# Performance work log

Hardware: AMD Instinct MI355X
Metric: run time of the kernel (lower is better)

## Reference

```python
import jax, jax.numpy as jnp
import numpy as np

BN_EPS = 1e-5
POOL_EPS = 1e-6


def conv3x3(x, w, b):
    # x: (N,C,H,W), w: (O,C,3,3) -> (N,O,H,W), stride 1, SAME padding
    y = jax.lax.conv_general_dilated(x, w, window_strides=(1, 1), padding='SAME',
                                     dimension_numbers=('NCHW', 'OIHW', 'NCHW'))
    return y + b[None, :, None, None]


def deform_conv2d(x, off_w, off_b, mod_w, mod_b, w, b):
    # Modulated deformable conv (DCNv2), 3x3, stride 1, padding 1 (torchvision semantics).
    N, C, H, W = x.shape
    off = conv3x3(x, off_w, off_b).reshape(N, 9, 2, H, W)  # per-tap (dy, dx)
    mod = 2.0 * jax.nn.sigmoid(conv3x3(x, mod_w, mod_b))   # (N,9,H,W)
    dy = (jnp.arange(3, dtype=x.dtype) - 1.0).repeat(3)    # tap k = ky*3+kx
    dx = jnp.tile(jnp.arange(3, dtype=x.dtype) - 1.0, 3)
    py = off[:, :, 0] + dy[None, :, None, None] + jnp.arange(H, dtype=x.dtype)[None, None, :, None]
    px = off[:, :, 1] + dx[None, :, None, None] + jnp.arange(W, dtype=x.dtype)[None, None, None, :]
    y0f = jnp.floor(py); x0f = jnp.floor(px)
    wy = py - y0f; wx = px - x0f
    y0 = y0f.astype(jnp.int32); x0 = x0f.astype(jnp.int32)
    flat = x.reshape(N, C, H * W)

    def gather(yi, xi):
        # zero padding outside the image
        valid = ((yi >= 0) & (yi < H) & (xi >= 0) & (xi < W)).astype(x.dtype)
        idx = jnp.clip(yi, 0, H - 1) * W + jnp.clip(xi, 0, W - 1)      # (N,9,H,W)
        idx_b = jnp.broadcast_to(idx.reshape(N, 1, -1), (N, C, 9 * H * W))
        g = jnp.take_along_axis(flat, idx_b, axis=2).reshape(N, C, 9, H, W)
        return g * valid[:, None]

    s = (gather(y0, x0) * ((1 - wy) * (1 - wx))[:, None]
         + gather(y0, x0 + 1) * ((1 - wy) * wx)[:, None]
         + gather(y0 + 1, x0) * (wy * (1 - wx))[:, None]
         + gather(y0 + 1, x0 + 1) * (wy * wx)[:, None])       # (N,C,9,H,W)
    out = jnp.einsum('nckij,nkij,ock->noij', s, mod, w.reshape(w.shape[0], C, 9))
    return out + b[None, :, None, None]


def setup_inputs() -> dict:
    key = jax.random.key(0)
    ks = jax.random.split(key, 20)
    b, n_f, n_i, Hm, Wm = 2, 8, 10, 192, 192
    C_in, C_dcn, n_inc, n_pix = 256, 64, 128, 64
    h, w = 96, 96
    f32 = jnp.float32
    inp = {
        'x': jax.random.normal(ks[0], (b * n_f, C_in, h, w), f32),
        'masks': jax.random.uniform(ks[1], (b, n_f, n_i, Hm, Wm), f32),
        'conv1_w': jax.random.normal(ks[2], (C_dcn, C_in, 3, 3), f32) * 0.02,
        'conv1_b': jnp.zeros((C_dcn,), f32),
        'bn_gamma': jnp.ones((C_dcn,), f32),
        'bn_beta': jnp.zeros((C_dcn,), f32),
        'bn_mean': jax.random.normal(ks[3], (C_dcn,), f32) * 0.01,
        'bn_var': jnp.ones((C_dcn,), f32),
        'off_w': jax.random.normal(ks[4], (18, C_dcn, 3, 3), f32) * 0.01,
        'off_b': jnp.zeros((18,), f32),
        'mod_w': jax.random.normal(ks[5], (9, C_dcn, 3, 3), f32) * 0.01,
        'mod_b': jnp.zeros((9,), f32),
        'dcn_w': jax.random.normal(ks[6], (C_dcn, C_dcn, 3, 3), f32) * 0.05,
        'dcn_b': jnp.zeros((C_dcn,), f32),
        'smooth_w': jax.random.normal(ks[7], (C_dcn, C_dcn), f32) * 0.05,
        'smooth_b': jnp.zeros((C_dcn,), f32),
        'inc_w': jax.random.normal(ks[8], (n_inc, C_dcn), f32) * 0.05,
        'pix_w': jax.random.normal(ks[9], (n_pix, C_dcn), f32) * 0.05,
    }
    return inp


def reference(x, masks, conv1_w, conv1_b, bn_gamma, bn_beta, bn_mean, bn_var,
              off_w, off_b, mod_w, mod_b, dcn_w, dcn_b,
              smooth_w, smooth_b, inc_w, pix_w):
    # conv1: Conv3x3 + BatchNorm (eval stats) + ReLU
    y = conv3x3(x, conv1_w, conv1_b)
    y = (y - bn_mean[None, :, None, None]) * (bn_gamma[None, :, None, None]
        * jax.lax.rsqrt(bn_var + BN_EPS)[None, :, None, None]) + bn_beta[None, :, None, None]
    y = jax.nn.relu(y)
    # deformable conv
    y = deform_conv2d(y, off_w, off_b, mod_w, mod_b, dcn_w, dcn_b)

    b, n_f, n_i, Hm, Wm = masks.shape
    N, C, h, w = y.shape
    # resizeAnyShape -> bilinear, align_corners=False
    m = jax.image.resize(masks.reshape(b * n_f * n_i, Hm, Wm),
                         (b * n_f * n_i, h, w), method='bilinear', antialias=False)
    m = m.reshape(b, n_f, n_i, h * w)
    xf = y.reshape(b, n_f, C, h * w)
    # mask-weighted spatial average: avoid (b,n_f,n_i,C,h*w) intermediate
    num = jnp.einsum('bfcp,bfip->bfic', xf, m)            # (b,n_f,n_i,C)
    den = m.sum(axis=-1)[..., None]                        # (b,n_f,n_i,1)
    feat = num / (den + POOL_EPS)
    feat = jax.nn.relu(feat @ smooth_w.T + smooth_b)
    inc_kernels = feat @ inc_w.T
    pix_kernels = feat @ pix_w.T
    return (inc_kernels, pix_kernels)
```

## Files before the change

### kernel.cpp

```cpp
#include <hip/hip_runtime.h>
#include <hip/hip_bf16.h>

typedef __attribute__((ext_vector_type(8))) __bf16 bf16x8;
typedef __attribute__((ext_vector_type(4))) float f32x4;
typedef __attribute__((ext_vector_type(4))) unsigned int u32x4;
typedef __attribute__((ext_vector_type(2))) unsigned int u32x2;
typedef __attribute__((ext_vector_type(4))) unsigned short u16x4;
typedef __attribute__((ext_vector_type(8))) unsigned short ushort8;

#define MFMA16(a,b,c) __builtin_amdgcn_mfma_f32_16x16x32_bf16((a),(b),(c),0,0,0)

__device__ __forceinline__ float b2f(unsigned short u) {
  union { unsigned int i; float f; } v; v.i = ((unsigned int)u) << 16; return v.f;
}
__device__ __forceinline__ unsigned short f2b(float f) {
  union { float f; unsigned int u; } v; v.f = f;
  unsigned int u = v.u;
  unsigned int r = (u + 0x7fffu + ((u >> 16) & 1u)) >> 16;
  return (unsigned short)r;
}
__device__ __forceinline__ unsigned short f2h(float f) {
  _Float16 x = (_Float16)f; unsigned short r; __builtin_memcpy(&r, &x, 2); return r;
}
__device__ __forceinline__ float h2f(unsigned short h) {
  _Float16 x; __builtin_memcpy(&x, &h, 2); return (float)x;
}

#define NIMG 16
#define CIN  256
#define CD   64
#define HH   96
#define WW   96
#define HW   (HH*WW)

#define OFF_Y1   (0ll)
#define OFF_Y2   (18874368ll)
#define OFF_OFF  (37748736ll)
#define OFF_MOD  (48365568ll)
#define OFF_M    (53673984ll)
#define OFF_NP   OFF_OFF
#define OFF_DP   (OFF_OFF + 1310720ll)
#define OFF_SBN  (59908096ll)
#define OFF_TBN  (59908352ll)
#define OFF_W1   (59908608ll)
#define OFF_W2   (60203520ll)
#define OFF_W3   (60240384ll)
#define WS_NEEDED (60314112ll)

__global__ void k_prep(const float* __restrict__ conv1_w, const float* __restrict__ conv1_b,
                       const float* __restrict__ bn_gamma, const float* __restrict__ bn_beta,
                       const float* __restrict__ bn_mean, const float* __restrict__ bn_var,
                       const float* __restrict__ off_w, const float* __restrict__ mod_w,
                       const float* __restrict__ dcn_w,
                       unsigned short* __restrict__ w1, unsigned short* __restrict__ w2,
                       unsigned short* __restrict__ w3,
                       float* __restrict__ sbn, float* __restrict__ tbn)
{
  int e = blockIdx.x * 256 + threadIdx.x;
  if (e < 147456) {
    int j = e & 7, o = (e >> 3) & 63, cg = (e >> 9) & 31, t = e >> 14;
    w1[e] = f2b(conv1_w[(o * 256 + cg * 8 + j) * 9 + t]);
  } else if (e < 147456 + 18432) {
    int i = e - 147456;
    int j = i & 7, o = (i >> 3) & 31, cg = (i >> 8) & 7, t = i >> 11;
    int ch = cg * 8 + j;
    float v = 0.f;
    if (o < 18)      v = off_w[(o * 64 + ch) * 9 + t];
    else if (o < 27) v = mod_w[((o - 18) * 64 + ch) * 9 + t];
    w2[i] = f2b(v);
  } else if (e < 147456 + 18432 + 36864) {
    int i = e - 147456 - 18432;
    int j = i & 7, o = (i >> 3) & 63, cg = (i >> 9) & 7, t = i >> 12;
    w3[i] = f2b(dcn_w[(o * 64 + cg * 8 + j) * 9 + t]);
  } else {
    int i = e - (147456 + 18432 + 36864);
    if (i < 64) {
      sbn[i] = bn_gamma[i] * rsqrtf(bn_var[i] + 1e-5f);
    } else if (i < 128) {
      int q = i - 64;
      float s = bn_gamma[q] * rsqrtf(bn_var[q] + 1e-5f);
      tbn[q] = (conv1_b[q] - bn_mean[q]) * s + bn_beta[q];
    }
  }
}

__global__ __launch_bounds__(256)
void k_tr(const float* __restrict__ x, unsigned short* __restrict__ xT, int n_base)
{
  __shared__ __align__(16) unsigned short ls[64][68];
  const int tid = threadIdx.x;
  const int p0 = blockIdx.x * 64, c0 = blockIdx.y * 64, nl = blockIdx.z;
  const float* xn = x + (size_t)(n_base + nl) * CIN * HW;

  const int p4 = tid & 15, cb = tid >> 4;
  #pragma unroll
  for (int it = 0; it < 4; ++it) {
    int c = cb + it * 16;
    f32x4 v = *reinterpret_cast<const f32x4*>(xn + (size_t)(c0 + c) * HW + p0 + p4 * 4);
    #pragma unroll
    for (int q = 0; q < 4; ++q) ls[p4 * 4 + q][c] = f2b(v[q]);
  }
  __syncthreads();
  const int cg = tid & 7, pb = tid >> 3;
  #pragma unroll
  for (int it = 0; it < 2; ++it) {
    int p = pb + it * 32;
    u32x2 lo = *reinterpret_cast<const u32x2*>(&ls[p][cg * 8]);
    u32x2 hi = *reinterpret_cast<const u32x2*>(&ls[p][cg * 8 + 4]);
    u32x4 v = {lo[0], lo[1], hi[0], hi[1]};
    *reinterpret_cast<u32x4*>(&xT[((size_t)nl * HW + p0 + p) * CIN + c0 + cg * 8]) = v;
  }
}

__global__ __launch_bounds__(256)
void k_conv1t(const unsigned short* __restrict__ xT, const unsigned short* __restrict__ w1,
              const float* __restrict__ sbn, const float* __restrict__ tbn,
              unsigned short* __restrict__ y1, int n_base)
{
  __shared__ __align__(16) unsigned short xs[4][98][40];

  const int tid = threadIdx.x;
  const int lane = tid & 63, wv = tid >> 6;
  const int l16 = lane & 15, lg = lane >> 4;
  const int wrow = wv & 1, wch = wv >> 1;
  const int h0 = blockIdx.x * 2;
  const int nl = blockIdx.y;
  const int n = n_base + nl;
  const unsigned short* xn = xT + (size_t)nl * HW * CIN;

  f32x4 acc[2][6];
  #pragma unroll
  for (int a = 0; a < 2; ++a)
    #pragma unroll
    for (int b = 0; b < 6; ++b) { f32x4 z = {0.f,0.f,0.f,0.f}; acc[a][b] = z; }

  for (int chunk = 0; chunk < 8; ++chunk) {
    const int c0 = chunk * 32;
    __syncthreads();
    #pragma unroll
    for (int it = 0; it < 6; ++it) {
      int idx = tid + it * 256;
      int cg = idx & 3, w = (idx >> 2) % 96, r = idx / 384;
      int row = h0 - 1 + r;
      u32x4 v = {0u,0u,0u,0u};
      if (row >= 0 && row < HH)
        v = *reinterpret_cast<const u32x4*>(&xn[((size_t)row * WW + w) * CIN + c0 + cg * 8]);
      *reinterpret_cast<u32x4*>(&xs[r][w + 1][cg * 8]) = v;
    }
    if (tid < 32) {
      int r = tid >> 3, side = (tid >> 2) & 1, cg = tid & 3;
      u32x4 z = {0u,0u,0u,0u};
      *reinterpret_cast<u32x4*>(&xs[r][side * 97][cg * 8]) = z;
    }
    __syncthreads();
    #pragma unroll
    for (int t = 0; t < 9; ++t) {
      const int ky = t / 3, kx = t % 3;
      bf16x8 a0 = *reinterpret_cast<const bf16x8*>(
          &w1[((t * 32 + chunk * 4 + lg) * 64 + wch * 32 + l16) * 8]);
      bf16x8 a1 = *reinterpret_cast<const bf16x8*>(
          &w1[((t * 32 + chunk * 4 + lg) * 64 + wch * 32 + 16 + l16) * 8]);
      const int r = wrow + ky;
      #pragma unroll
      for (int wt = 0; wt < 6; ++wt) {
        bf16x8 b = *reinterpret_cast<const bf16x8*>(&xs[r][wt*16 + l16 + kx][lg*8]);
        acc[0][wt] = MFMA16(a0, b, acc[0][wt]);
        acc[1][wt] = MFMA16(a1, b, acc[1][wt]);
      }
    }
  }
  __syncthreads();
  unsigned short* ys = &xs[0][0][0];
  #pragma unroll
  for (int ct = 0; ct < 2; ++ct) {
    int o4 = wch * 32 + ct * 16 + lg * 4;
    f32x4 s4 = *reinterpret_cast<const f32x4*>(&sbn[o4]);
    f32x4 t4 = *reinterpret_cast<const f32x4*>(&tbn[o4]);
    #pragma unroll
    for (int wt = 0; wt < 6; ++wt) {
      int p = wrow * 96 + wt * 16 + l16;
      float v0 = acc[ct][wt][0] * s4[0] + t4[0]; v0 = v0 > 0.f ? v0 : 0.f;
      float v1 = acc[ct][wt][1] * s4[1] + t4[1]; v1 = v1 > 0.f ? v1 : 0.f;
      float v2 = acc[ct][wt][2] * s4[2] + t4[2]; v2 = v2 > 0.f ? v2 : 0.f;
      float v3 = acc[ct][wt][3] * s4[3] + t4[3]; v3 = v3 > 0.f ? v3 : 0.f;
      u32x2 d = {(unsigned)f2b(v0) | ((unsigned)f2b(v1) << 16),
                 (unsigned)f2b(v2) | ((unsigned)f2b(v3) << 16)};
      *reinterpret_cast<u32x2*>(&ys[p * 72 + o4]) = d;
    }
  }
  __syncthreads();
  #pragma unroll
  for (int it = 0; it < 6; ++it) {
    int idx = tid + it * 256;
    int cg = idx & 7, p = (idx >> 3) % 96, r = idx / 768;
    *reinterpret_cast<u32x4*>(&y1[(((size_t)n * HH + h0 + r) * WW + p) * CD + cg * 8]) =
      *reinterpret_cast<const u32x4*>(&ys[(r * 96 + p) * 72 + cg * 8]);
  }
}

__global__ __launch_bounds__(256)
void k_conv2(const unsigned short* __restrict__ y1, const unsigned short* __restrict__ w2,
             const float* __restrict__ off_b, const float* __restrict__ mod_b,
             float* __restrict__ off_o, float* __restrict__ mod_o)
{
  __shared__ __align__(16) unsigned short xs[4][98][40];

  const int tid = threadIdx.x;
  const int lane = tid & 63, wv = tid >> 6;
  const int l16 = lane & 15, lg = lane >> 4;
  const int wrow = wv & 1, wct = wv >> 1;
  const int h0 = blockIdx.x * 2;
  const int n = blockIdx.y;
  const unsigned short* y1n = y1 + (size_t)n * HW * CD;

  f32x4 acc[6];
  #pragma unroll
  for (int b = 0; b < 6; ++b) { f32x4 z = {0.f,0.f,0.f,0.f}; acc[b] = z; }

  #pragma unroll
  for (int chunk = 0; chunk < 2; ++chunk) {
    const int c0 = chunk * 32;
    bf16x8 aR[9];
    #pragma unroll
    for (int t = 0; t < 9; ++t)
      aR[t] = *reinterpret_cast<const bf16x8*>(
          &w2[((t * 8 + chunk * 4 + lg) * 32 + wct * 16 + l16) * 8]);
    __syncthreads();
    #pragma unroll
    for (int it = 0; it < 6; ++it) {
      int idx = tid + it * 256;
      int cg = idx & 3, w = (idx >> 2) % 96, r = idx / 384;
      int row = h0 - 1 + r;
      u32x4 v = {0u,0u,0u,0u};
      if (row >= 0 && row < HH)
        v = *reinterpret_cast<const u32x4*>(&y1n[((size_t)row * WW + w) * CD + c0 + cg * 8]);
      *reinterpret_cast<u32x4*>(&xs[r][w + 1][cg * 8]) = v;
    }
    if (tid < 32) {
      int r = tid >> 3, side = (tid >> 2) & 1, cg = tid & 3;
      u32x4 z = {0u,0u,0u,0u};
      *reinterpret_cast<u32x4*>(&xs[r][side * 97][cg * 8]) = z;
    }
    __syncthreads();
    #pragma unroll
    for (int t = 0; t < 9; ++t) {
      const int ky = t / 3, kx = t % 3;
      const int r = wrow + ky;
      #pragma unroll
      for (int wt = 0; wt < 6; ++wt) {
        bf16x8 b = *reinterpret_cast<const bf16x8*>(&xs[r][wt*16 + l16 + kx][lg*8]);
        acc[wt] = MFMA16(aR[t], b, acc[wt]);
      }
    }
  }
  const int h = h0 + wrow;
  #pragma unroll
  for (int j = 0; j < 4; ++j) {
    int o = wct * 16 + lg * 4 + j;
    if (o < 18) {
      float bo = off_b[o];
      #pragma unroll
      for (int wt = 0; wt < 6; ++wt)
        off_o[((n * 18 + o) * HH + h) * WW + wt * 16 + l16] = acc[wt][j] + bo;
    } else if (o < 27) {
      int q = o - 18;
      float bo = mod_b[q];
      #pragma unroll
      for (int wt = 0; wt < 6; ++wt) {
        float v = acc[wt][j] + bo;
        mod_o[((n * 9 + q) * HH + h) * WW + wt * 16 + l16] = 2.f / (1.f + expf(-v));
      }
    }
  }
}

__global__ __launch_bounds__(256)
void k_dcn(const unsigned short* __restrict__ y1, const float* __restrict__ off_i,
           const float* __restrict__ mod_i, const unsigned short* __restrict__ w3g,
           const float* __restrict__ dcn_b, unsigned short* __restrict__ y2)
{
  __shared__ __align__(16) unsigned short meta[864][8];
  __shared__ __align__(16) unsigned short Bs[96][72];

  const int tid = threadIdx.x;
  const int lane = tid & 63, wv = tid >> 6;
  const int l16 = lane & 15, lg = lane >> 4;
  const int h = blockIdx.x, n = blockIdx.y;

  #pragma unroll
  for (int it = 0; it < 4; ++it) {
    int e = tid + it * 256;
    if (e < 864) {
      int k = e / 96, p = e % 96;
      float dy = off_i[((n * 18 + 2 * k) * HH + h) * WW + p];
      float dx = off_i[((n * 18 + 2 * k + 1) * HH + h) * WW + p];
      float mw = mod_i[((n * 9 + k) * HH + h) * WW + p];
      float py = (float)(h + k / 3 - 1) + dy;
      float px = (float)(p + k % 3 - 1) + dx;
      float y0f = floorf(py), x0f = floorf(px);
      float wy = py - y0f, wx = px - x0f;
      int iy0 = (int)y0f, ix0 = (int)x0f;
      int iy1 = iy0 + 1, ix1 = ix0 + 1;
      float vy0 = (iy0 >= 0 && iy0 < HH) ? 1.f : 0.f;
      float vy1 = (iy1 >= 0 && iy1 < HH) ? 1.f : 0.f;
      float vx0 = (ix0 >= 0 && ix0 < WW) ? 1.f : 0.f;
      float vx1 = (ix1 >= 0 && ix1 < WW) ? 1.f : 0.f;
      unsigned short m0 = f2h((1.f - wy) * (1.f - wx) * mw * vy0 * vx0);
      unsigned short m1 = f2h((1.f - wy) * wx         * mw * vy0 * vx1);
      unsigned short m2 = f2h(wy         * (1.f - wx) * mw * vy1 * vx0);
      unsigned short m3 = f2h(wy         * wx         * mw * vy1 * vx1);
      int cy0 = iy0 < 0 ? 0 : (iy0 > 95 ? 95 : iy0);
      int cy1 = iy1 < 0 ? 0 : (iy1 > 95 ? 95 : iy1);
      int cx0 = ix0 < 0 ? 0 : (ix0 > 95 ? 95 : ix0);
      int cx1 = ix1 < 0 ? 0 : (ix1 > 95 ? 95 : ix1);
      u32x4 pk = {(unsigned)m0 | ((unsigned)m1 << 16),
                  (unsigned)m2 | ((unsigned)m3 << 16),
                  (unsigned)(cy0 * WW + cx0) | ((unsigned)(cy0 * WW + cx1) << 16),
                  (unsigned)(cy1 * WW + cx0) | ((unsigned)(cy1 * WW + cx1) << 16)};
      *reinterpret_cast<u32x4*>(&meta[e][0]) = pk;
    }
  }
  __syncthreads();

  const unsigned short* y1n = y1 + (size_t)n * HW * CD;
  f32x4 acc[6];
  #pragma unroll
  for (int b = 0; b < 6; ++b) { f32x4 z = {0.f,0.f,0.f,0.f}; acc[b] = z; }

  #pragma unroll
  for (int t = 0; t < 9; ++t) {
    bf16x8 a0 = *reinterpret_cast<const bf16x8*>(
        &w3g[((t * 8 + lg) * 64 + wv * 16 + l16) * 8]);
    bf16x8 a1 = *reinterpret_cast<const bf16x8*>(
        &w3g[((t * 8 + 4 + lg) * 64 + wv * 16 + l16) * 8]);
    #pragma unroll
    for (int it = 0; it < 3; ++it) {
      int idx = tid + it * 256;
      int cg = idx & 7, p = idx >> 3;
      u32x4 mk = *reinterpret_cast<const u32x4*>(&meta[t * 96 + p][0]);
      float hw0 = h2f((unsigned short)(mk[0] & 0xffffu));
      float hw1 = h2f((unsigned short)(mk[0] >> 16));
      float hw2 = h2f((unsigned short)(mk[1] & 0xffffu));
      float hw3 = h2f((unsigned short)(mk[1] >> 16));
      int o0 = (int)(mk[2] & 0xffffu) << 6;
      int o1 = (int)(mk[2] >> 16) << 6;
      int o2 = (int)(mk[3] & 0xffffu) << 6;
      int o3 = (int)(mk[3] >> 16) << 6;
      ushort8 g0 = *reinterpret_cast<const ushort8*>(&y1n[o0 + cg * 8]);
      ushort8 g1 = *reinterpret_cast<const ushort8*>(&y1n[o1 + cg * 8]);
      ushort8 g2 = *reinterpret_cast<const ushort8*>(&y1n[o2 + cg * 8]);
      ushort8 g3 = *reinterpret_cast<const ushort8*>(&y1n[o3 + cg * 8]);
      unsigned int wds[4];
      #pragma unroll
      for (int q = 0; q < 4; ++q) {
        float va = hw0*b2f(g0[2*q])   + hw1*b2f(g1[2*q])
                 + hw2*b2f(g2[2*q])   + hw3*b2f(g3[2*q]);
        float vb = hw0*b2f(g0[2*q+1]) + hw1*b2f(g1[2*q+1])
                 + hw2*b2f(g2[2*q+1]) + hw3*b2f(g3[2*q+1]);
        wds[q] = (unsigned int)f2b(va) | ((unsigned int)f2b(vb) << 16);
      }
      u32x4 pk = {wds[0], wds[1], wds[2], wds[3]};
      *reinterpret_cast<u32x4*>(&Bs[p][cg * 8]) = pk;
    }
    __syncthreads();
    #pragma unroll
    for (int wt = 0; wt < 6; ++wt) {
      bf16x8 b0 = *reinterpret_cast<const bf16x8*>(&Bs[wt * 16 + l16][lg * 8]);
      bf16x8 b1 = *reinterpret_cast<const bf16x8*>(&Bs[wt * 16 + l16][32 + lg * 8]);
      acc[wt] = MFMA16(a0, b0, acc[wt]);
      acc[wt] = MFMA16(a1, b1, acc[wt]);
    }
    __syncthreads();
  }

  unsigned short* Bs2 = &Bs[0][0];
  {
    int o4 = wv * 16 + lg * 4;
    f32x4 b4 = *reinterpret_cast<const f32x4*>(&dcn_b[o4]);
    #pragma unroll
    for (int wt = 0; wt < 6; ++wt) {
      int p = wt * 16 + l16;
      u32x2 d = {(unsigned)f2b(acc[wt][0] + b4[0]) | ((unsigned)f2b(acc[wt][1] + b4[1]) << 16),
                 (unsigned)f2b(acc[wt][2] + b4[2]) | ((unsigned)f2b(acc[wt][3] + b4[3]) << 16)};
      *reinterpret_cast<u32x2*>(&Bs2[p * 72 + o4]) = d;
    }
  }
  __syncthreads();
  #pragma unroll
  for (int it = 0; it < 3; ++it) {
    int idx = tid + it * 256;
    int cg = idx & 7, p = idx >> 3;
    *reinterpret_cast<u32x4*>(&y2[(((size_t)n * HH + h) * WW + p) * CD + cg * 8]) =
      *reinterpret_cast<const u32x4*>(&Bs2[p * 72 + cg * 8]);
  }
}

__global__ void k_resize(const float* __restrict__ masks, float* __restrict__ m)
{
  int gid = blockIdx.x * 256 + threadIdx.x;
  if (gid >= 16 * 10 * HW) return;
  int pix = gid % HW;
  int r = gid / HW;
  int oh = pix / WW, ow = pix % WW;
  const float* s = masks + ((size_t)r * 192 + 2 * oh) * 192 + 2 * ow;
  m[gid] = 0.25f * (s[0] + s[1] + s[192] + s[193]);
}

__global__ __launch_bounds__(256)
void k_pool(const unsigned short* __restrict__ y2, const float* __restrict__ m,
            float* __restrict__ num_part, float* __restrict__ den_part)
{
  __shared__ float ms[10][288];
  __shared__ float red[4][10][64];
  __shared__ float den_red[10][16];
  const int tid = threadIdx.x;
  const int seg = blockIdx.x, bf = blockIdx.y;
  const int p0 = seg * 288;

  #pragma unroll
  for (int it = 0; it < 12; ++it) {
    int idx = tid + it * 256;
    if (idx < 2880) {
      int i = idx / 288, p = idx % 288;
      ms[i][p] = m[(bf * 10 + i) * HW + p0 + p];
    }
  }
  __syncthreads();

  const int c = tid & 63, grp = tid >> 6;
  float acc[10];
  #pragma unroll
  for (int i = 0; i < 10; ++i) acc[i] = 0.f;
  const unsigned short* yb = y2 + ((size_t)bf * HW + p0 + grp * 72) * CD + c;
  for (int p = 0; p < 72; ++p) {
    float v = b2f(yb[p * CD]);
    #pragma unroll
    for (int i = 0; i < 10; ++i) acc[i] += v * ms[i][grp * 72 + p];
  }
  #pragma unroll
  for (int i = 0; i < 10; ++i) red[grp][i][c] = acc[i];
  if (tid < 160) {
    int i = tid >> 4, s16 = tid & 15;
    float s = 0.f;
    for (int k2 = 0; k2 < 18; ++k2) s += ms[i][s16 + k2 * 16];
    den_red[i][s16] = s;
  }
  __syncthreads();
  #pragma unroll
  for (int it = 0; it < 3; ++it) {
    int e = tid + it * 256;
    if (e < 640) {
      int i = e >> 6, cc = e & 63;
      num_part[((bf * 32 + seg) * 10 + i) * 64 + cc] =
        red[0][i][cc] + red[1][i][cc] + red[2][i][cc] + red[3][i][cc];
    }
  }
  if (tid < 10) {
    float s = 0.f;
    for (int k2 = 0; k2 < 16; ++k2) s += den_red[tid][k2];
    den_part[(bf * 32 + seg) * 16 + tid] = s;
  }
}

__global__ void k_head(const float* __restrict__ num_part, const float* __restrict__ den_part,
                       const float* __restrict__ smooth_w, const float* __restrict__ smooth_b,
                       const float* __restrict__ inc_w, const float* __restrict__ pix_w,
                       float* __restrict__ out)
{
  __shared__ float pool_s[10][64];
  __shared__ float feat_s[10][64];
  const int tid = threadIdx.x;
  const int bf = blockIdx.x;
  #pragma unroll
  for (int it = 0; it < 3; ++it) {
    int e = tid + it * 256;
    if (e < 640) {
      int i = e >> 6, cc = e & 63;
      float nsum = 0.f, dsum = 0.f;
      for (int s = 0; s < 32; ++s) {
        nsum += num_part[((bf * 32 + s) * 10 + i) * 64 + cc];
        dsum += den_part[(bf * 32 + s) * 16 + i];
      }
      pool_s[i][cc] = nsum / (dsum + 1e-6f);
    }
  }
  __syncthreads();
  #pragma unroll
  for (int it = 0; it < 3; ++it) {
    int e = tid + it * 256;
    if (e < 640) {
      int i = e >> 6, cc = e & 63;
      float s = smooth_b[cc];
      for (int k = 0; k < 64; ++k) s += pool_s[i][k] * smooth_w[cc * 64 + k];
      feat_s[i][cc] = s > 0.f ? s : 0.f;
    }
  }
  __syncthreads();
  #pragma unroll
  for (int it = 0; it < 5; ++it) {
    int e = tid + it * 256;
    if (e < 1280) {
      int i = e >> 7, oc = e & 127;
      float s = 0.f;
      for (int k = 0; k < 64; ++k) s += feat_s[i][k] * inc_w[oc * 64 + k];
      out[(bf * 10 + i) * 128 + oc] = s;
    }
  }
  #pragma unroll
  for (int it = 0; it < 3; ++it) {
    int e = tid + it * 256;
    if (e < 640) {
      int i = e >> 6, oc = e & 63;
      float s = 0.f;
      for (int k = 0; k < 64; ++k) s += feat_s[i][k] * pix_w[oc * 64 + k];
      out[20480 + (bf * 10 + i) * 64 + oc] = s;
    }
  }
}

extern "C" void kernel_launch(void* const* d_in, const int* in_sizes, int n_in,
                              void* d_out, int out_size, void* d_ws, size_t ws_size,
                              hipStream_t stream)
{
  const float* x        = (const float*)d_in[0];
  const float* masks    = (const float*)d_in[1];
  const float* conv1_w  = (const float*)d_in[2];
  const float* conv1_b  = (const float*)d_in[3];
  const float* bn_gamma = (const float*)d_in[4];
  const float* bn_beta  = (const float*)d_in[5];
  const float* bn_mean  = (const float*)d_in[6];
  const float* bn_var   = (const float*)d_in[7];
  const float* off_w    = (const float*)d_in[8];
  const float* off_b    = (const float*)d_in[9];
  const float* mod_w    = (const float*)d_in[10];
  const float* mod_b    = (const float*)d_in[11];
  const float* dcn_w    = (const float*)d_in[12];
  const float* dcn_b    = (const float*)d_in[13];
  const float* smooth_w = (const float*)d_in[14];
  const float* smooth_b = (const float*)d_in[15];
  const float* inc_w    = (const float*)d_in[16];
  const float* pix_w    = (const float*)d_in[17];
  float* out = (float*)d_out;

  if (ws_size < (size_t)WS_NEEDED) return;
  char* ws = (char*)d_ws;
  unsigned short* y1  = (unsigned short*)(ws + OFF_Y1);
  unsigned short* y2  = (unsigned short*)(ws + OFF_Y2);
  unsigned short* xT  = (unsigned short*)(ws + OFF_Y2);
  float* off_t        = (float*)(ws + OFF_OFF);
  float* mod_t        = (float*)(ws + OFF_MOD);
  float* mbuf         = (float*)(ws + OFF_M);
  float* num_part     = (float*)(ws + OFF_NP);
  float* den_part     = (float*)(ws + OFF_DP);
  float* sbn          = (float*)(ws + OFF_SBN);
  float* tbn          = (float*)(ws + OFF_TBN);
  unsigned short* w1  = (unsigned short*)(ws + OFF_W1);
  unsigned short* w2  = (unsigned short*)(ws + OFF_W2);
  unsigned short* w3  = (unsigned short*)(ws + OFF_W3);

  k_prep<<<793, 256, 0, stream>>>(conv1_w, conv1_b, bn_gamma, bn_beta, bn_mean, bn_var,
                                  off_w, mod_w, dcn_w, w1, w2, w3, sbn, tbn);
  for (int pass = 0; pass < 2; ++pass) {
    int n_base = pass * 8;
    k_tr<<<dim3(144, 4, 8), 256, 0, stream>>>(x, xT, n_base);
    k_conv1t<<<dim3(48, 8), 256, 0, stream>>>(xT, w1, sbn, tbn, y1, n_base);
  }
  k_conv2<<<dim3(48, 16), 256, 0, stream>>>(y1, w2, off_b, mod_b, off_t, mod_t);
  k_dcn<<<dim3(96, 16), 256, 0, stream>>>(y1, off_t, mod_t, w3, dcn_b, y2);
  k_resize<<<(16 * 10 * HW + 255) / 256, 256, 0, stream>>>(masks, mbuf);
  k_pool<<<dim3(32, 16), 256, 0, stream>>>(y2, mbuf, num_part, den_part);
  k_head<<<16, 256, 0, stream>>>(num_part, den_part, smooth_w, smooth_b, inc_w, pix_w, out);
}
```

Before: 486.3 us.

## Split conv1 into one-row blocks, vectorize resize, and double pool segments

Result: no change. 478.4 us (-1.6%).

```diff
diff --git a/kernel.cpp b/kernel.cpp
--- a/kernel.cpp
+++ b/kernel.cpp
@@ -3,6 +3,7 @@
 
 typedef __attribute__((ext_vector_type(8))) __bf16 bf16x8;
 typedef __attribute__((ext_vector_type(4))) float f32x4;
+typedef __attribute__((ext_vector_type(2))) float f32x2;
 typedef __attribute__((ext_vector_type(4))) unsigned int u32x4;
 typedef __attribute__((ext_vector_type(2))) unsigned int u32x2;
 typedef __attribute__((ext_vector_type(4))) unsigned short u16x4;
@@ -39,7 +40,7 @@
 #define OFF_MOD  (48365568ll)
 #define OFF_M    (53673984ll)
 #define OFF_NP   OFF_OFF
-#define OFF_DP   (OFF_OFF + 1310720ll)
+#define OFF_DP   (OFF_OFF + 2621440ll)
 #define OFF_SBN  (59908096ll)
 #define OFF_TBN  (59908352ll)
 #define OFF_W1   (59908608ll)
@@ -117,40 +118,43 @@
               const float* __restrict__ sbn, const float* __restrict__ tbn,
               unsigned short* __restrict__ y1, int n_base)
 {
-  __shared__ __align__(16) unsigned short xs[4][98][40];
+  __shared__ __align__(16) unsigned short sbuf[3 * 98 * 40];
+  #define XS(r,w,c) sbuf[((r) * 98 + (w)) * 40 + (c)]
 
   const int tid = threadIdx.x;
   const int lane = tid & 63, wv = tid >> 6;
   const int l16 = lane & 15, lg = lane >> 4;
-  const int wrow = wv & 1, wch = wv >> 1;
-  const int h0 = blockIdx.x * 2;
+  const int wch = wv & 1, wpx = wv >> 1;
+  const int h = blockIdx.x;
   const int nl = blockIdx.y;
   const int n = n_base + nl;
   const unsigned short* xn = xT + (size_t)nl * HW * CIN;
 
-  f32x4 acc[2][6];
+  f32x4 acc[2][3];
   #pragma unroll
   for (int a = 0; a < 2; ++a)
     #pragma unroll
-    for (int b = 0; b < 6; ++b) { f32x4 z = {0.f,0.f,0.f,0.f}; acc[a][b] = z; }
+    for (int b = 0; b < 3; ++b) { f32x4 z = {0.f,0.f,0.f,0.f}; acc[a][b] = z; }
 
   for (int chunk = 0; chunk < 8; ++chunk) {
     const int c0 = chunk * 32;
     __syncthreads();
     #pragma unroll
-    for (int it = 0; it < 6; ++it) {
+    for (int it = 0; it < 5; ++it) {
       int idx = tid + it * 256;
-      int cg = idx & 3, w = (idx >> 2) % 96, r = idx / 384;
-      int row = h0 - 1 + r;
-      u32x4 v = {0u,0u,0u,0u};
-      if (row >= 0 && row < HH)
-        v = *reinterpret_cast<const u32x4*>(&xn[((size_t)row * WW + w) * CIN + c0 + cg * 8]);
-      *reinterpret_cast<u32x4*>(&xs[r][w + 1][cg * 8]) = v;
-    }
-    if (tid < 32) {
+      if (idx < 1152) {
+        int cg = idx & 3, w = (idx >> 2) % 96, r = idx / 384;
+        int row = h - 1 + r;
+        u32x4 v = {0u,0u,0u,0u};
+        if (row >= 0 && row < HH)
+          v = *reinterpret_cast<const u32x4*>(&xn[((size_t)row * WW + w) * CIN + c0 + cg * 8]);
+        *reinterpret_cast<u32x4*>(&XS(r, w + 1, cg * 8)) = v;
+      }
+    }
+    if (tid < 24) {
       int r = tid >> 3, side = (tid >> 2) & 1, cg = tid & 3;
       u32x4 z = {0u,0u,0u,0u};
-      *reinterpret_cast<u32x4*>(&xs[r][side * 97][cg * 8]) = z;
+      *reinterpret_cast<u32x4*>(&XS(r, side * 97, cg * 8)) = z;
     }
     __syncthreads();
     #pragma unroll
@@ -160,25 +164,24 @@
           &w1[((t * 32 + chunk * 4 + lg) * 64 + wch * 32 + l16) * 8]);
       bf16x8 a1 = *reinterpret_cast<const bf16x8*>(
           &w1[((t * 32 + chunk * 4 + lg) * 64 + wch * 32 + 16 + l16) * 8]);
-      const int r = wrow + ky;
       #pragma unroll
-      for (int wt = 0; wt < 6; ++wt) {
-        bf16x8 b = *reinterpret_cast<const bf16x8*>(&xs[r][wt*16 + l16 + kx][lg*8]);
+      for (int wt = 0; wt < 3; ++wt) {
+        bf16x8 b = *reinterpret_cast<const bf16x8*>(&XS(ky, wpx*48 + wt*16 + l16 + kx, lg*8));
         acc[0][wt] = MFMA16(a0, b, acc[0][wt]);
         acc[1][wt] = MFMA16(a1, b, acc[1][wt]);
       }
     }
   }
   __syncthreads();
-  unsigned short* ys = &xs[0][0][0];
+  unsigned short* ys = &sbuf[0];
   #pragma unroll
   for (int ct = 0; ct < 2; ++ct) {
     int o4 = wch * 32 + ct * 16 + lg * 4;
     f32x4 s4 = *reinterpret_cast<const f32x4*>(&sbn[o4]);
     f32x4 t4 = *reinterpret_cast<const f32x4*>(&tbn[o4]);
     #pragma unroll
-    for (int wt = 0; wt < 6; ++wt) {
-      int p = wrow * 96 + wt * 16 + l16;
+    for (int wt = 0; wt < 3; ++wt) {
+      int p = wpx * 48 + wt * 16 + l16;
       float v0 = acc[ct][wt][0] * s4[0] + t4[0]; v0 = v0 > 0.f ? v0 : 0.f;
       float v1 = acc[ct][wt][1] * s4[1] + t4[1]; v1 = v1 > 0.f ? v1 : 0.f;
       float v2 = acc[ct][wt][2] * s4[2] + t4[2]; v2 = v2 > 0.f ? v2 : 0.f;
@@ -190,12 +193,13 @@
   }
   __syncthreads();
   #pragma unroll
-  for (int it = 0; it < 6; ++it) {
+  for (int it = 0; it < 3; ++it) {
     int idx = tid + it * 256;
-    int cg = idx & 7, p = (idx >> 3) % 96, r = idx / 768;
-    *reinterpret_cast<u32x4*>(&y1[(((size_t)n * HH + h0 + r) * WW + p) * CD + cg * 8]) =
-      *reinterpret_cast<const u32x4*>(&ys[(r * 96 + p) * 72 + cg * 8]);
-  }
+    int cg = idx & 7, p = idx >> 3;
+    *reinterpret_cast<u32x4*>(&y1[(((size_t)n * HH + h) * WW + p) * CD + cg * 8]) =
+      *reinterpret_cast<const u32x4*>(&ys[p * 72 + cg * 8]);
+  }
+  #undef XS
 }
 
 __global__ __launch_bounds__(256)
@@ -398,51 +402,63 @@
 __global__ void k_resize(const float* __restrict__ masks, float* __restrict__ m)
 {
   int gid = blockIdx.x * 256 + threadIdx.x;
-  if (gid >= 16 * 10 * HW) return;
-  int pix = gid % HW;
-  int r = gid / HW;
-  int oh = pix / WW, ow = pix % WW;
-  const float* s = masks + ((size_t)r * 192 + 2 * oh) * 192 + 2 * ow;
-  m[gid] = 0.25f * (s[0] + s[1] + s[192] + s[193]);
+  if (gid >= 16 * 10 * HH * 48) return;
+  int ow2 = (gid % 48) * 2;
+  int oh = (gid / 48) % HH;
+  int r = gid / (48 * HH);
+  const float* s = masks + ((size_t)r * 192 + 2 * oh) * 192 + 2 * ow2;
+  f32x4 v0 = *reinterpret_cast<const f32x4*>(s);
+  f32x4 v1 = *reinterpret_cast<const f32x4*>(s + 192);
+  f32x2 o = {0.25f * (v0[0] + v0[1] + v1[0] + v1[1]),
+             0.25f * (v0[2] + v0[3] + v1[2] + v1[3])};
+  *reinterpret_cast<f32x2*>(&m[(size_t)r * HW + oh * WW + ow2]) = o;
 }
 
 __global__ __launch_bounds__(256)
 void k_pool(const unsigned short* __restrict__ y2, const float* __restrict__ m,
             float* __restrict__ num_part, float* __restrict__ den_part)
 {
-  __shared__ float ms[10][288];
+  __shared__ float ms2[144][12];
   __shared__ float red[4][10][64];
   __shared__ float den_red[10][16];
   const int tid = threadIdx.x;
   const int seg = blockIdx.x, bf = blockIdx.y;
-  const int p0 = seg * 288;
-
-  #pragma unroll
-  for (int it = 0; it < 12; ++it) {
+  const int p0 = seg * 144;
+
+  #pragma unroll
+  for (int it = 0; it < 6; ++it) {
     int idx = tid + it * 256;
-    if (idx < 2880) {
-      int i = idx / 288, p = idx % 288;
-      ms[i][p] = m[(bf * 10 + i) * HW + p0 + p];
+    if (idx < 1440) {
+      int i = idx / 144, p = idx % 144;
+      ms2[p][i] = m[(bf * 10 + i) * HW + p0 + p];
     }
   }
   __syncthreads();
 
   const int c = tid & 63, grp = tid >> 6;
-  float acc[10];
-  #pragma unroll
-  for (int i = 0; i < 10; ++i) acc[i] = 0.f;
-  const unsigned short* yb = y2 + ((size_t)bf * HW + p0 + grp * 72) * CD + c;
-  for (int p = 0; p < 72; ++p) {
+  f32x2 acc2[5];
+  #pragma unroll
+  for (int i = 0; i < 5; ++i) { f32x2 z = {0.f, 0.f}; acc2[i] = z; }
+  const unsigned short* yb = y2 + ((size_t)bf * HW + p0 + grp * 36) * CD + c;
+  for (int p = 0; p < 36; ++p) {
     float v = b2f(yb[p * CD]);
-    #pragma unroll
-    for (int i = 0; i < 10; ++i) acc[i] += v * ms[i][grp * 72 + p];
-  }
-  #pragma unroll
-  for (int i = 0; i < 10; ++i) red[grp][i][c] = acc[i];
+    f32x2 vv = {v, v};
+    int pp = grp * 36 + p;
+    #pragma unroll
+    for (int i2 = 0; i2 < 5; ++i2) {
+      f32x2 mp = *reinterpret_cast<const f32x2*>(&ms2[pp][i2 * 2]);
+      acc2[i2] += vv * mp;
+    }
+  }
+  #pragma unroll
+  for (int i2 = 0; i2 < 5; ++i2) {
+    red[grp][2 * i2 + 0][c] = acc2[i2][0];
+    red[grp][2 * i2 + 1][c] = acc2[i2][1];
+  }
   if (tid < 160) {
     int i = tid >> 4, s16 = tid & 15;
     float s = 0.f;
-    for (int k2 = 0; k2 < 18; ++k2) s += ms[i][s16 + k2 * 16];
+    for (int k2 = 0; k2 < 9; ++k2) s += ms2[s16 + k2 * 16][i];
     den_red[i][s16] = s;
   }
   __syncthreads();
@@ -451,14 +467,14 @@
     int e = tid + it * 256;
     if (e < 640) {
       int i = e >> 6, cc = e & 63;
-      num_part[((bf * 32 + seg) * 10 + i) * 64 + cc] =
+      num_part[((bf * 64 + seg) * 10 + i) * 64 + cc] =
         red[0][i][cc] + red[1][i][cc] + red[2][i][cc] + red[3][i][cc];
     }
   }
   if (tid < 10) {
     float s = 0.f;
     for (int k2 = 0; k2 < 16; ++k2) s += den_red[tid][k2];
-    den_part[(bf * 32 + seg) * 16 + tid] = s;
+    den_part[(bf * 64 + seg) * 16 + tid] = s;
   }
 }
 
@@ -477,9 +493,9 @@
     if (e < 640) {
       int i = e >> 6, cc = e & 63;
       float nsum = 0.f, dsum = 0.f;
-      for (int s = 0; s < 32; ++s) {
-        nsum += num_part[((bf * 32 + s) * 10 + i) * 64 + cc];
-        dsum += den_part[(bf * 32 + s) * 16 + i];
+      for (int s = 0; s < 64; ++s) {
+        nsum += num_part[((bf * 64 + s) * 10 + i) * 64 + cc];
+        dsum += den_part[(bf * 64 + s) * 16 + i];
       }
       pool_s[i][cc] = nsum / (dsum + 1e-6f);
     }
@@ -563,11 +579,11 @@
   for (int pass = 0; pass < 2; ++pass) {
     int n_base = pass * 8;
     k_tr<<<dim3(144, 4, 8), 256, 0, stream>>>(x, xT, n_base);
-    k_conv1t<<<dim3(48, 8), 256, 0, stream>>>(xT, w1, sbn, tbn, y1, n_base);
+    k_conv1t<<<dim3(96, 8), 256, 0, stream>>>(xT, w1, sbn, tbn, y1, n_base);
   }
   k_conv2<<<dim3(48, 16), 256, 0, stream>>>(y1, w2, off_b, mod_b, off_t, mod_t);
   k_dcn<<<dim3(96, 16), 256, 0, stream>>>(y1, off_t, mod_t, w3, dcn_b, y2);
-  k_resize<<<(16 * 10 * HW + 255) / 256, 256, 0, stream>>>(masks, mbuf);
-  k_pool<<<dim3(32, 16), 256, 0, stream>>>(y2, mbuf, num_part, den_part);
+  k_resize<<<(16 * 10 * HH * 48 + 255) / 256, 256, 0, stream>>>(masks, mbuf);
+  k_pool<<<dim3(64, 16), 256, 0, stream>>>(y2, mbuf, num_part, den_part);
   k_head<<<16, 256, 0, stream>>>(num_part, den_part, smooth_w, smooth_b, inc_w, pix_w, out);
 }
```
